# Kernel tuning notes

Measured on AMD Instinct MI355X. Metric: run time of the kernel, lower is better.

The kernel has to match this reference:

```python
import jax, jax.numpy as jnp
import numpy as np

N = 65536      # total nodes (ground + sub)
NG = 32768     # ground nodes (subnodes are NG..N)
H = 64         # n_hidden
FIN = 32       # n_node_features
L = 2          # num_convolution_blocks
B = 64         # graphs in batch
MAXDEG = 10    # MFConv max_degree -> 11 buckets
EG = 1048576   # ground-graph edges
ES = 1048576   # subgraph edges
EX = 524288    # cross (ground<->sub) edges


def setup_inputs() -> dict:
    key = jax.random.key(0)
    ks = jax.random.split(key, 32)
    NS = N - NG
    x = jax.random.normal(ks[0], (N, FIN), jnp.float32)
    # ground graph: src/dst in [0, NG)
    edge_index = jax.random.randint(ks[1], (2, EG), 0, NG).astype(jnp.int64)
    # subgraph: src/dst in [NG, N)
    subgraph_edge_index = (NG + jax.random.randint(ks[2], (2, ES), 0, NS)).astype(jnp.int64)
    # ground -> sub
    ns_src = jax.random.randint(ks[3], (EX,), 0, NG)
    ns_dst = NG + jax.random.randint(ks[4], (EX,), 0, NS)
    node_subnode_index = jnp.stack([ns_src, ns_dst]).astype(jnp.int64)
    # sub -> ground
    sn_src = NG + jax.random.randint(ks[5], (EX,), 0, NS)
    sn_dst = jax.random.randint(ks[6], (EX,), 0, NG)
    subnode_node_index = jnp.stack([sn_src, sn_dst]).astype(jnp.int64)
    ground_node = jnp.arange(N) < NG
    subgraph_batch_index = jax.random.randint(ks[7], (N,), 0, B).astype(jnp.int64)
    batch_idx = jax.random.randint(ks[8], (N,), 0, B).astype(jnp.int64)
    s = 0.05
    p = {}
    p['embed_W'] = jax.random.normal(ks[9], (FIN, H), jnp.float32) * s
    p['embed_b'] = jnp.zeros((H,), jnp.float32)
    names = ['ground', 'g2s', 'sub', 's2g']
    for i, nm in enumerate(names):
        p[nm + '_Wl'] = jax.random.normal(ks[10 + 3 * i], (L, MAXDEG + 1, H, H), jnp.float32) * s
        p[nm + '_bl'] = jnp.zeros((L, MAXDEG + 1, H), jnp.float32)
        p[nm + '_Wr'] = jax.random.normal(ks[11 + 3 * i], (L, MAXDEG + 1, H, H), jnp.float32) * s
    p['W1'] = jax.random.normal(ks[24], (H, H), jnp.float32) * s
    p['b1'] = jnp.zeros((H,), jnp.float32)
    p['W2'] = jax.random.normal(ks[25], (H, 1), jnp.float32) * s
    p['b2'] = jnp.zeros((1,), jnp.float32)
    return dict(x=x, edge_index=edge_index, subgraph_edge_index=subgraph_edge_index,
                node_subnode_index=node_subnode_index, subnode_node_index=subnode_node_index,
                ground_node=ground_node, subgraph_batch_index=subgraph_batch_index,
                batch_idx=batch_idx, **p)


def _mfconv(h, src, dst, Wl, bl, Wr):
    # PyG MFConv: out_i = Lin_l[deg_i](sum_{j->i} h_j) + Lin_r[deg_i](h_i), deg clamped to MAXDEG
    n = h.shape[0]
    deg = jnp.clip(jax.ops.segment_sum(jnp.ones(src.shape[0], jnp.int32), dst, num_segments=n), 0, MAXDEG)
    agg = jax.ops.segment_sum(h[src], dst, num_segments=n)  # [n, H] sum aggregation
    out = jnp.zeros((n, Wl.shape[-1]), h.dtype)
    for d in range(MAXDEG + 1):
        m = (deg == d)[:, None]
        out = out + jnp.where(m, agg @ Wl[d] + bl[d] + h @ Wr[d], jnp.zeros((), h.dtype))
    return out


def _masked_conv(h, ei, Wl, bl, Wr):
    # nodes that never receive a message keep their old features (catch_lone_sender)
    src, dst = ei[0], ei[1]
    recv = jnp.zeros((h.shape[0],), bool).at[dst].set(True)
    return jnp.where(recv[:, None], _mfconv(h, src, dst, Wl, bl, Wr), h)


def reference(x, edge_index, subgraph_edge_index, node_subnode_index, subnode_node_index,
              ground_node, subgraph_batch_index, batch_idx,
              embed_W, embed_b,
              ground_Wl, ground_bl, ground_Wr,
              g2s_Wl, g2s_bl, g2s_Wr,
              sub_Wl, sub_bl, sub_Wr,
              s2g_Wl, s2g_bl, s2g_Wr,
              W1, b1, W2, b2):
    h = x @ embed_W + embed_b
    for l in range(L):
        if l > 0:
            h = jax.nn.relu(h)
        h = _masked_conv(h, edge_index, ground_Wl[l], ground_bl[l], ground_Wr[l])
        h = _masked_conv(h, node_subnode_index, g2s_Wl[l], g2s_bl[l], g2s_Wr[l])
        h = _masked_conv(h, subgraph_edge_index, sub_Wl[l], sub_bl[l], sub_Wr[l])
        h = _masked_conv(h, subnode_node_index, s2g_Wl[l], s2g_bl[l], s2g_Wr[l])
    # global_add_pool over ground nodes only
    pooled = jax.ops.segment_sum(jnp.where(ground_node[:, None], h, jnp.zeros((), h.dtype)),
                                 batch_idx, num_segments=B)  # [B, H]
    z = jax.nn.relu(pooled @ W1 + b1)
    return z @ W2 + b2  # [B, 1]
```

## Files before the change

kernel.cpp:

```cpp
#include <hip/hip_runtime.h>

#define N_NODES 65536
#define NGROUND 32768
#define NHALF 32768
#define H 64
#define FIN 32
#define NB 64
#define MAXDEG 10
#define RSTRIDE 32769
#define EG 1048576
#define ES 1048576
#define EX 524288
#define TE (EG + EX + ES + EX)
#define BIN2 512
#define NPB 64
#define CHUNK 8192
#define TC 384
#define CNT_LEN 196608
#define NSCANB 192
#define BCAP 6144
#define NEB 2048
#define NFB 32
#define ESTR 80

typedef __attribute__((ext_vector_type(8))) short short8;
typedef __attribute__((ext_vector_type(4))) float f32x4;
typedef unsigned short u16;
typedef unsigned int u32;

__device__ __forceinline__ u16 f2bf(float x) {
    unsigned int u = __float_as_uint(x);
    unsigned int r = u + 0x7FFFu + ((u >> 16) & 1u);
    return (u16)(r >> 16);
}
__device__ __forceinline__ float bf2f(u16 b) {
    return __uint_as_float(((unsigned int)b) << 16);
}
__device__ __forceinline__ u32 relu2(u32 w) {
    u32 lo = w & 0xFFFFu;
    if (lo & 0x8000u) lo = 0;
    u32 hi = w >> 16;
    if (hi & 0x8000u) hi = 0;
    return lo | (hi << 16);
}

__device__ __forceinline__ void chunk_resolve(int b, int& set, int& cin,
                                              int& nc, int& base, int& dbase, int& sbase) {
    if (b < 128)      { set = 0; cin = b;       nc = 128; base = 0;      dbase = 0;       sbase = 0; }
    else if (b < 192) { set = 1; cin = b - 128; nc = 64;  base = 65536;  dbase = NGROUND; sbase = 0; }
    else if (b < 320) { set = 2; cin = b - 192; nc = 128; base = 98304;  dbase = NGROUND; sbase = NGROUND; }
    else              { set = 3; cin = b - 320; nc = 64;  base = 163840; dbase = 0;       sbase = NGROUND; }
}

__global__ __launch_bounds__(256) void embed_prep_count_kernel(
    const float* __restrict__ x, const float* __restrict__ W,
    const float* __restrict__ b, u16* __restrict__ hgHi, u16* __restrict__ hsHi,
    const float* W0l, const float* W0r, const float* W1l, const float* W1r,
    const float* W2l, const float* W2r, const float* W3l, const float* W3r,
    short8* __restrict__ fragbuf,
    const int* __restrict__ d0, const int* __restrict__ d1,
    const int* __restrict__ d2, const int* __restrict__ d3,
    int* __restrict__ cnt) {
    int tid = threadIdx.x;
    if (blockIdx.x >= NEB + NFB) {
        __shared__ int hist[BIN2];
        int set, cin, nc, base, dbase, sbase;
        chunk_resolve(blockIdx.x - NEB - NFB, set, cin, nc, base, dbase, sbase);
        const int* dp = set == 0 ? d0 : set == 1 ? d1 : set == 2 ? d2 : d3;
        for (int i = tid; i < BIN2; i += 256) hist[i] = 0;
        __syncthreads();
        int e0 = cin * CHUNK;
        for (int i = tid; i < CHUNK; i += 256) {
            int d = __builtin_nontemporal_load(&dp[e0 + i]) - dbase;
            atomicAdd(&hist[d >> 6], 1);
        }
        __syncthreads();
        for (int i = tid; i < BIN2; i += 256)
            cnt[base + i * nc + cin] = hist[i];
        return;
    }
    if (blockIdx.x >= NEB) {
        int tid2 = (blockIdx.x - NEB) * 256 + tid;
        int lane = tid2 & 63;
        int f8 = (tid2 >> 6) & 7;
        int mat = (tid2 >> 9) & 1;
        int layer = (tid2 >> 10) & 1;
        int set = (tid2 >> 11) & 3;
        int s = f8 >> 2, t = f8 & 3;
        const float* Wb;
        if (set == 0) Wb = mat ? W0r : W0l;
        else if (set == 1) Wb = mat ? W1r : W1l;
        else if (set == 2) Wb = mat ? W2r : W2l;
        else Wb = mat ? W3r : W3l;
        Wb += ((size_t)layer * (MAXDEG + 1) + MAXDEG) * H * H;
        int k0 = s * 32 + (lane >> 4) * 8;
        int n = t * 16 + (lane & 15);
        short8 hi, lo;
#pragma unroll
        for (int j = 0; j < 8; j++) {
            float w = Wb[(size_t)(k0 + j) * H + n];
            u16 hb = f2bf(w);
            u16 lb = f2bf(w - bf2f(hb));
            hi[j] = (short)hb;
            lo[j] = (short)lb;
        }
        size_t basehi = ((size_t)(((set * 2 + layer) * 2 + mat) * 2 + 0) * 8 + f8) * 64 + lane;
        size_t baselo = ((size_t)(((set * 2 + layer) * 2 + mat) * 2 + 1) * 8 + f8) * 64 + lane;
        fragbuf[basehi] = hi;
        fragbuf[baselo] = lo;
        return;
    }
    int f = tid & 63;
    int wy = tid >> 6;
    __shared__ float sW[FIN * H];
    for (int i = tid; i < FIN * H; i += 256) sW[i] = W[i];
    __syncthreads();
    float bf_ = b[f];
#pragma unroll
    for (int it = 0; it < 8; it++) {
        int node = blockIdx.x * 32 + it * 4 + wy;
        const float* xr = x + (size_t)node * FIN;
        float acc = bf_;
#pragma unroll
        for (int k = 0; k < FIN; k++) acc += xr[k] * sW[k * H + f];
        if (node < NGROUND)
            hgHi[(size_t)node * H + f] = f2bf(acc);
        else
            hsHi[(size_t)(node - NGROUND) * H + f] = f2bf(acc);
    }
}

__global__ __launch_bounds__(256) void scanA_kernel(
    int* __restrict__ cnt, int* __restrict__ bsum) {
    __shared__ int lds[256];
    int t = threadIdx.x;
    int base = blockIdx.x * 1024 + t * 4;
    int v0 = cnt[base], v1 = cnt[base + 1], v2 = cnt[base + 2], v3 = cnt[base + 3];
    int s = v0 + v1 + v2 + v3;
    lds[t] = s;
    __syncthreads();
    for (int d = 1; d < 256; d <<= 1) {
        int x = 0;
        if (t >= d) x = lds[t - d];
        __syncthreads();
        lds[t] += x;
        __syncthreads();
    }
    int pref = lds[t] - s;
    cnt[base] = pref;
    cnt[base + 1] = pref + v0;
    cnt[base + 2] = pref + v0 + v1;
    cnt[base + 3] = pref + v0 + v1 + v2;
    if (t == 255) bsum[blockIdx.x] = pref + s;
}

__global__ __launch_bounds__(256) void scanB_kernel(int* __restrict__ bsum) {
    __shared__ int lds[256];
    int t = threadIdx.x;
    int v = (t < NSCANB) ? bsum[t] : 0;
    lds[t] = v;
    __syncthreads();
    for (int d = 1; d < 256; d <<= 1) {
        int x = 0;
        if (t >= d) x = lds[t - d];
        __syncthreads();
        lds[t] += x;
        __syncthreads();
    }
    if (t < NSCANB) bsum[t] = lds[t] - v;
}

__global__ __launch_bounds__(256) void partition_kernel(
    const int* __restrict__ s0, const int* __restrict__ s1,
    const int* __restrict__ s2, const int* __restrict__ s3,
    const int* __restrict__ d0, const int* __restrict__ d1,
    const int* __restrict__ d2, const int* __restrict__ d3,
    const int* __restrict__ cnt, const int* __restrict__ bsum,
    u32* __restrict__ csru) {
    __shared__ u32 buf[CHUNK];
    __shared__ int hist[BIN2];
    __shared__ int lofs[BIN2];
    __shared__ int gbase[BIN2];
    __shared__ int sc[256];
    int set, cin, nc, base, dbase, sbase;
    chunk_resolve(blockIdx.x, set, cin, nc, base, dbase, sbase);
    const int* dp = set == 0 ? d0 : set == 1 ? d1 : set == 2 ? d2 : d3;
    const int* sp = set == 0 ? s0 : set == 1 ? s1 : set == 2 ? s2 : s3;
    int t = threadIdx.x;
    for (int i = t; i < BIN2; i += 256) hist[i] = 0;
    __syncthreads();
    u32 pk[32];
    int e0 = cin * CHUNK;
#pragma unroll
    for (int j = 0; j < 32; j++) {
        int idx = e0 + t + j * 256;
        int d = __builtin_nontemporal_load(&dp[idx]) - dbase;
        int s = __builtin_nontemporal_load(&sp[idx]) - sbase;
        pk[j] = ((u32)d << 15) | (u32)s;
        atomicAdd(&hist[d >> 6], 1);
    }
    __syncthreads();
    int h0 = hist[2 * t], h1 = hist[2 * t + 1];
    int hs = h0 + h1;
    sc[t] = hs;
    __syncthreads();
    for (int d2 = 1; d2 < 256; d2 <<= 1) {
        int v = 0;
        if (t >= d2) v = sc[t - d2];
        __syncthreads();
        sc[t] += v;
        __syncthreads();
    }
    int pref = sc[t] - hs;
    lofs[2 * t] = pref;
    lofs[2 * t + 1] = pref + h0;
    hist[2 * t] = pref;
    hist[2 * t + 1] = pref + h0;
    for (int i = t; i < BIN2; i += 256) {
        int idx = base + i * nc + cin;
        gbase[i] = cnt[idx] + bsum[idx >> 10];
    }
    __syncthreads();
#pragma unroll
    for (int j = 0; j < 32; j++) {
        int bin = pk[j] >> 21;
        int pos = atomicAdd(&hist[bin], 1);
        buf[pos] = pk[j];
    }
    __syncthreads();
    for (int i = t; i < CHUNK; i += 256) {
        u32 pkt = buf[i];
        int d = pkt >> 15;
        int bin = d >> 6;
        int gpos = gbase[bin] + (i - lofs[bin]);
        csru[gpos] = pkt & 0x1FFFFFu;
    }
}

__global__ __launch_bounds__(256) void finalize_kernel(
    u32* __restrict__ csru, const int* __restrict__ cnt,
    const int* __restrict__ bsum, int* __restrict__ rowstart4) {
    __shared__ u32 buf[BCAP];
    __shared__ int deg[NPB], off[NPB];
    int b = blockIdx.x;
    int set = b >> 9, bin = b & 511;
    int nc = (set == 0 || set == 2) ? 128 : 64;
    int base = set == 0 ? 0 : set == 1 ? 65536 : set == 2 ? 98304 : 163840;
    int flat = base + bin * nc;
    int binstart = cnt[flat] + bsum[flat >> 10];
    int binend = (b == 2047) ? TE : (cnt[flat + nc] + bsum[(flat + nc) >> 10]);
    int n = binend - binstart;
    for (int i = threadIdx.x; i < n; i += 256) buf[i] = csru[binstart + i];
    if (threadIdx.x < NPB) deg[threadIdx.x] = 0;
    __syncthreads();
    for (int i = threadIdx.x; i < n; i += 256) atomicAdd(&deg[buf[i] >> 15], 1);
    __syncthreads();
    if (threadIdx.x == 0) {
        int r = 0;
        for (int j = 0; j < NPB; j++) { off[j] = r; r += deg[j]; }
    }
    __syncthreads();
    int coffset = set == 0 ? 0 : set == 1 ? EG : set == 2 ? EG + EX : EG + EX + ES;
    if (threadIdx.x < NPB)
        rowstart4[set * RSTRIDE + bin * NPB + threadIdx.x] =
            binstart - coffset + off[threadIdx.x];
    if (bin == 0 && threadIdx.x == 0)
        rowstart4[set * RSTRIDE + NHALF] = (set == 0 || set == 2) ? EG : EX;
    if (threadIdx.x < NPB) deg[threadIdx.x] = off[threadIdx.x];
    __syncthreads();
    for (int i = threadIdx.x; i < n; i += 256) {
        u32 pkt = buf[i];
        int dl = pkt >> 15;
        int pos = atomicAdd(&deg[dl], 1);
        csru[binstart + pos] = pkt & 0x7FFFu;
    }
}

__global__ __launch_bounds__(256) void conv_fused_kernel(
    const u16* __restrict__ srcHi, const u16* __restrict__ selfHi,
    u16* __restrict__ outHi, const int* __restrict__ csr,
    const int* __restrict__ rowstart, const short8* __restrict__ fragbase,
    const float* __restrict__ Wlp, const float* __restrict__ Wrp,
    const float* __restrict__ blp, int do_relu, u32* __restrict__ relu_buf) {
    if (blockIdx.x >= 2048) {
        int base = ((blockIdx.x - 2048) * 256 + threadIdx.x) * 2;
        uint4* p = (uint4*)relu_buf;
        uint4 a = p[base], b = p[base + 1];
        a.x = relu2(a.x); a.y = relu2(a.y); a.z = relu2(a.z); a.w = relu2(a.w);
        b.x = relu2(b.x); b.y = relu2(b.y); b.z = relu2(b.z); b.w = relu2(b.w);
        p[base] = a;
        p[base + 1] = b;
        return;
    }
    __shared__ u16 sB[H][ESTR];
    __shared__ float sAgg[16][68];
    int tid = threadIdx.x;
    int w = tid >> 6, lane = tid & 63;
    int node0 = blockIdx.x * 16;
    int q = lane >> 4, mrow = lane & 15;

    int R0 = rowstart[node0];
    int R16 = rowstart[node0 + 16];
    int rlo = rowstart[node0 + mrow];
    int rhi = rowstart[node0 + mrow + 1];
    u32 rspan = (u32)(rhi - rlo);

    f32x4 aggv = (f32x4){0.f, 0.f, 0.f, 0.f};

    int el = lane;
    int fh = w;
    for (int ce = R0; ce < R16; ce += 64) {
        int eg = ce + el;
        int src = csr[min(eg, R16 - 1)];
        const uint4* rp = (const uint4*)(srcHi + (size_t)src * H + fh * 16);
        uint4 va = rp[0];
        uint4 vb = rp[1];
        __syncthreads();
        u32 wa[4] = {va.x, va.y, va.z, va.w};
        u32 wb[4] = {vb.x, vb.y, vb.z, vb.w};
#pragma unroll
        for (int k = 0; k < 4; k++) {
            sB[fh * 16 + 2 * k][el] = (u16)wa[k];
            sB[fh * 16 + 2 * k + 1][el] = (u16)(wa[k] >> 16);
            sB[fh * 16 + 8 + 2 * k][el] = (u16)wb[k];
            sB[fh * 16 + 8 + 2 * k + 1][el] = (u16)(wb[k] >> 16);
        }
        __syncthreads();
#pragma unroll
        for (int half = 0; half < 2; half++) {
            int kb = ce + half * 32 + q * 8;
            short8 Af;
#pragma unroll
            for (int j = 0; j < 8; j++) {
                u32 off = (u32)(kb + j) - (u32)rlo;
                Af[j] = (off < rspan) ? (short)0x3F80 : (short)0;
            }
            short8 Bf = *(const short8*)&sB[w * 16 + mrow][half * 32 + q * 8];
            aggv = __builtin_amdgcn_mfma_f32_16x16x32_bf16(Af, Bf, aggv, 0, 0, 0);
        }
    }
#pragma unroll
    for (int r = 0; r < 4; r++) sAgg[q * 4 + r][w * 16 + mrow] = aggv[r];
    __syncthreads();

    int myrow = node0 + mrow;
    int mydeg = rhi - rlo;
    unsigned long long ball = __ballot(min(mydeg, MAXDEG) != MAXDEG);
    unsigned exc = (unsigned)(ball & 0xFFFFull);
    int t = w;

    f32x4 accv = (f32x4){0.f, 0.f, 0.f, 0.f};
    const short8* fb = fragbase + lane;
#pragma unroll
    for (int s = 0; s < 2; s++) {
        float av[8];
        *(float4*)&av[0] = *(const float4*)&sAgg[mrow][s * 32 + q * 8];
        *(float4*)&av[4] = *(const float4*)&sAgg[mrow][s * 32 + q * 8 + 4];
        short8 Ahi;
#pragma unroll
        for (int j = 0; j < 8; j++) Ahi[j] = (short)f2bf(av[j]);
        short8 Hhi = *(const short8*)(selfHi + (size_t)myrow * H + s * 32 + q * 8);
        short8 BLhi = fb[(size_t)((0 * 8) + s * 4 + t) * 64];
        short8 BLlo = fb[(size_t)((1 * 8) + s * 4 + t) * 64];
        short8 BRhi = fb[(size_t)((2 * 8) + s * 4 + t) * 64];
        short8 BRlo = fb[(size_t)((3 * 8) + s * 4 + t) * 64];
        accv = __builtin_amdgcn_mfma_f32_16x16x32_bf16(Ahi, BLhi, accv, 0, 0, 0);
        accv = __builtin_amdgcn_mfma_f32_16x16x32_bf16(Ahi, BLlo, accv, 0, 0, 0);
        accv = __builtin_amdgcn_mfma_f32_16x16x32_bf16(Hhi, BRhi, accv, 0, 0, 0);
        accv = __builtin_amdgcn_mfma_f32_16x16x32_bf16(Hhi, BRlo, accv, 0, 0, 0);
    }

    {
        int n = t * 16 + mrow;
        float bv = blp[MAXDEG * H + n];
#pragma unroll
        for (int r = 0; r < 4; r++) {
            int mm = q * 4 + r;
            if (!((exc >> mm) & 1)) {
                float val = accv[r] + bv;
                if (do_relu) val = fmaxf(val, 0.f);
                outHi[(size_t)(node0 + mm) * H + n] = f2bf(val);
            }
        }
    }

    if (exc & (0xFu << (w * 4))) {
        for (int i = 0; i < 4; i++) {
            int nr = w * 4 + i;
            if (!((exc >> nr) & 1)) continue;
            int node = node0 + nr;
            int st = rowstart[node], en = rowstart[node + 1];
            int dg = en - st;
            if (dg == 0) {
                float v = bf2f(selfHi[(size_t)node * H + lane]);
                if (do_relu) v = fmaxf(v, 0.f);
                outHi[(size_t)node * H + lane] = f2bf(v);
            } else {
                int d = min(dg, MAXDEG);
                const float* wl = Wlp + (size_t)d * H * H;
                const float* wr = Wrp + (size_t)d * H * H;
                float sval = bf2f(selfHi[(size_t)node * H + lane]);
                float o = blp[d * H + lane];
#pragma unroll 4
                for (int k = 0; k < H; k++) {
                    o += sAgg[nr][k] * wl[k * H + lane];
                    o += __shfl(sval, k, 64) * wr[k * H + lane];
                }
                if (do_relu) o = fmaxf(o, 0.f);
                outHi[(size_t)node * H + lane] = f2bf(o);
            }
        }
    }
}

__global__ __launch_bounds__(256) void pool_kernel(
    const u16* __restrict__ hgHi, const int* __restrict__ batch_idx,
    float* __restrict__ pooled) {
    __shared__ float lp[NB * H];
    int tid = threadIdx.x;
    for (int i = tid; i < NB * H; i += 256) lp[i] = 0.f;
    __syncthreads();
    int f = tid & 63;
    int wave = tid >> 6;
    int start = blockIdx.x * 64;
    for (int n = wave; n < 64; n += 4) {
        int node = start + n;
        int bi = batch_idx[node];
        atomicAdd(&lp[bi * H + f], bf2f(hgHi[(size_t)node * H + f]));
    }
    __syncthreads();
    for (int i = tid; i < NB * H; i += 256) {
        float v = lp[i];
        if (v != 0.f) atomicAdd(&pooled[i], v);
    }
}

__global__ __launch_bounds__(64) void mlp_kernel(
    const float* __restrict__ pooled, const float* __restrict__ W1,
    const float* __restrict__ b1, const float* __restrict__ W2,
    const float* __restrict__ b2, float* __restrict__ out) {
    int b = blockIdx.x;
    int j = threadIdx.x;
    const float* pr = pooled + b * H;
    float acc = b1[j];
#pragma unroll
    for (int k = 0; k < H; k++) acc += pr[k] * W1[k * H + j];
    acc = fmaxf(acc, 0.f);
    float v = acc * W2[j];
#pragma unroll
    for (int off = 32; off > 0; off >>= 1) v += __shfl_down(v, off, 64);
    if (j == 0) out[b] = v + b2[0];
}

extern "C" void kernel_launch(void* const* d_in, const int* in_sizes, int n_in,
                              void* d_out, int out_size, void* d_ws, size_t ws_size,
                              hipStream_t stream) {
    const float* x = (const float*)d_in[0];
    const int* ei_ground = (const int*)d_in[1];
    const int* ei_sub = (const int*)d_in[2];
    const int* ei_g2s = (const int*)d_in[3];
    const int* ei_s2g = (const int*)d_in[4];
    const int* batch_idx = (const int*)d_in[7];
    const float* embed_W = (const float*)d_in[8];
    const float* embed_b = (const float*)d_in[9];
    const float* Wl[4] = {(const float*)d_in[10], (const float*)d_in[13],
                          (const float*)d_in[16], (const float*)d_in[19]};
    const float* bl[4] = {(const float*)d_in[11], (const float*)d_in[14],
                          (const float*)d_in[17], (const float*)d_in[20]};
    const float* Wr[4] = {(const float*)d_in[12], (const float*)d_in[15],
                          (const float*)d_in[18], (const float*)d_in[21]};
    const float* W1 = (const float*)d_in[22];
    const float* b1 = (const float*)d_in[23];
    const float* W2 = (const float*)d_in[24];
    const float* b2 = (const float*)d_in[25];

    const int* s_[4] = {ei_ground, ei_g2s, ei_sub, ei_s2g};
    const int* dsr[4] = {ei_ground + EG, ei_g2s + EX, ei_sub + ES, ei_s2g + EX};
    const size_t coff[4] = {0, (size_t)EG, (size_t)EG + EX, (size_t)EG + EX + ES};

    const size_t HB = (size_t)NHALF * H * sizeof(u16);
    char* p = (char*)d_ws;
    u16* hgHi[2] = {(u16*)p, (u16*)(p + HB)};            p += 2 * HB;
    u16* hsHi[2] = {(u16*)p, (u16*)(p + HB)};            p += 2 * HB;
    u32* csru = (u32*)p;           p += (size_t)TE * sizeof(u32);
    int* cnt = (int*)p;            p += (size_t)CNT_LEN * sizeof(int);
    int* bsum = (int*)p;           p += (size_t)NSCANB * sizeof(int);
    int* rowstart4 = (int*)p;      p += (size_t)4 * RSTRIDE * sizeof(int);
    p += 16 - ((size_t)p & 15);
    short8* fragbuf = (short8*)p;  p += (size_t)8192 * sizeof(short8);
    float* pooled = (float*)p;

    embed_prep_count_kernel<<<NEB + NFB + TC, 256, 0, stream>>>(
        x, embed_W, embed_b, hgHi[0], hsHi[0],
        Wl[0], Wr[0], Wl[1], Wr[1], Wl[2], Wr[2], Wl[3], Wr[3], fragbuf,
        dsr[0], dsr[1], dsr[2], dsr[3], cnt);

    scanA_kernel<<<NSCANB, 256, 0, stream>>>(cnt, bsum);
    scanB_kernel<<<1, 256, 0, stream>>>(bsum);
    partition_kernel<<<TC, 256, 0, stream>>>(
        s_[0], s_[1], s_[2], s_[3], dsr[0], dsr[1], dsr[2], dsr[3], cnt, bsum, csru);
    finalize_kernel<<<2048, 256, 0, stream>>>(csru, cnt, bsum, rowstart4);
    const int* csr = (const int*)csru;

    int cg = 0, cs = 0;
    for (int l = 0; l < 2; l++) {
        for (int c = 0; c < 4; c++) {
            const u16 *srcHi, *selfHi;
            u16 *outHi;
            if (c == 0)      { srcHi = hgHi[cg]; selfHi = hgHi[cg]; outHi = hgHi[1 - cg]; }
            else if (c == 1) { srcHi = hgHi[cg]; selfHi = hsHi[cs]; outHi = hsHi[1 - cs]; }
            else if (c == 2) { srcHi = hsHi[cs]; selfHi = hsHi[cs]; outHi = hsHi[1 - cs]; }
            else             { srcHi = hsHi[cs]; selfHi = hgHi[cg]; outHi = hgHi[1 - cg]; }
            int do_relu = (l == 0 && c == 3) ? 1 : 0;
            int relu_blocks = (l == 1 && c == 0) ? 512 : 0;
            u32* relu_buf = (l == 1 && c == 0) ? (u32*)hsHi[cs] : (u32*)nullptr;
            conv_fused_kernel<<<2048 + relu_blocks, 256, 0, stream>>>(
                srcHi, selfHi, outHi,
                csr + coff[c], rowstart4 + (size_t)c * RSTRIDE,
                fragbuf + (size_t)(c * 2 + l) * 2048,
                Wl[c] + (size_t)l * (MAXDEG + 1) * H * H,
                Wr[c] + (size_t)l * (MAXDEG + 1) * H * H,
                bl[c] + (size_t)l * (MAXDEG + 1) * H, do_relu, relu_buf);
            if (c == 0 || c == 3) cg ^= 1; else cs ^= 1;
        }
    }

    hipMemsetAsync(pooled, 0, (size_t)NB * H * sizeof(float), stream);
    pool_kernel<<<NGROUND / 64, 256, 0, stream>>>(hgHi[cg], batch_idx, pooled);
    mlp_kernel<<<NB, 64, 0, stream>>>(pooled, W1, b1, W2, b2, (float*)d_out);
}
```

Baseline: 410.9 us.

## Double-buffer edge gather in conv kernel and replace pool atomics with partials

The conv aggregation loop now prefetches the next chunk's source indices and feature rows into registers while the current chunk is processed, and uses a double-buffered shared tile so only one barrier is needed per chunk. The shared row stride changes from 80 to 72. Pooling drops the memset and global atomics: 128 blocks each write a per-block partial, and the MLP kernel sums those partials before its matmul. This adds register pressure and shared memory in the conv kernel and extra partial-buffer traffic in the MLP.

```diff
diff --git a/kernel.cpp b/kernel.cpp
--- a/kernel.cpp
+++ b/kernel.cpp
@@ -21,7 +21,8 @@
 #define BCAP 6144
 #define NEB 2048
 #define NFB 32
-#define ESTR 80
+#define ESTR 72
+#define NPOOLB 128
 
 typedef __attribute__((ext_vector_type(8))) short short8;
 typedef __attribute__((ext_vector_type(4))) float f32x4;
@@ -292,7 +293,7 @@
         p[base + 1] = b;
         return;
     }
-    __shared__ u16 sB[H][ESTR];
+    __shared__ u16 sB[2][H][ESTR];
     __shared__ float sAgg[16][68];
     int tid = threadIdx.x;
     int w = tid >> 6, lane = tid & 63;
@@ -309,23 +310,32 @@
 
     int el = lane;
     int fh = w;
-    for (int ce = R0; ce < R16; ce += 64) {
-        int eg = ce + el;
-        int src = csr[min(eg, R16 - 1)];
-        const uint4* rp = (const uint4*)(srcHi + (size_t)src * H + fh * 16);
-        uint4 va = rp[0];
-        uint4 vb = rp[1];
-        __syncthreads();
-        u32 wa[4] = {va.x, va.y, va.z, va.w};
-        u32 wb[4] = {vb.x, vb.y, vb.z, vb.w};
+    int nch = (R16 - R0 + 63) >> 6;
+    int egb = R0 + el;
+
+    int sc_ = csr[min(egb, R16 - 1)];
+    const uint4* rp0 = (const uint4*)(srcHi + (size_t)sc_ * H + fh * 16);
+    uint4 va_c = rp0[0];
+    uint4 vb_c = rp0[1];
+    int sn_ = csr[min(egb + 64, R16 - 1)];
+
+    for (int t = 0; t < nch; t++) {
+        int cur = t & 1;
+        u32 wa[4] = {va_c.x, va_c.y, va_c.z, va_c.w};
+        u32 wb[4] = {vb_c.x, vb_c.y, vb_c.z, vb_c.w};
 #pragma unroll
         for (int k = 0; k < 4; k++) {
-            sB[fh * 16 + 2 * k][el] = (u16)wa[k];
-            sB[fh * 16 + 2 * k + 1][el] = (u16)(wa[k] >> 16);
-            sB[fh * 16 + 8 + 2 * k][el] = (u16)wb[k];
-            sB[fh * 16 + 8 + 2 * k + 1][el] = (u16)(wb[k] >> 16);
-        }
-        __syncthreads();
+            sB[cur][fh * 16 + 2 * k][el] = (u16)wa[k];
+            sB[cur][fh * 16 + 2 * k + 1][el] = (u16)(wa[k] >> 16);
+            sB[cur][fh * 16 + 8 + 2 * k][el] = (u16)wb[k];
+            sB[cur][fh * 16 + 8 + 2 * k + 1][el] = (u16)(wb[k] >> 16);
+        }
+        const uint4* rpn = (const uint4*)(srcHi + (size_t)sn_ * H + fh * 16);
+        uint4 va_n = rpn[0];
+        uint4 vb_n = rpn[1];
+        int sn2_ = csr[min(egb + (t + 2) * 64, R16 - 1)];
+        __syncthreads();
+        int ce = R0 + (t << 6);
 #pragma unroll
         for (int half = 0; half < 2; half++) {
             int kb = ce + half * 32 + q * 8;
@@ -335,9 +345,10 @@
                 u32 off = (u32)(kb + j) - (u32)rlo;
                 Af[j] = (off < rspan) ? (short)0x3F80 : (short)0;
             }
-            short8 Bf = *(const short8*)&sB[w * 16 + mrow][half * 32 + q * 8];
+            short8 Bf = *(const short8*)&sB[cur][w * 16 + mrow][half * 32 + q * 8];
             aggv = __builtin_amdgcn_mfma_f32_16x16x32_bf16(Af, Bf, aggv, 0, 0, 0);
         }
+        va_c = va_n; vb_c = vb_n; sn_ = sn2_;
     }
 #pragma unroll
     for (int r = 0; r < 4; r++) sAgg[q * 4 + r][w * 16 + mrow] = aggv[r];
@@ -415,33 +426,36 @@
 
 __global__ __launch_bounds__(256) void pool_kernel(
     const u16* __restrict__ hgHi, const int* __restrict__ batch_idx,
-    float* __restrict__ pooled) {
+    float* __restrict__ partials) {
     __shared__ float lp[NB * H];
     int tid = threadIdx.x;
     for (int i = tid; i < NB * H; i += 256) lp[i] = 0.f;
     __syncthreads();
     int f = tid & 63;
     int wave = tid >> 6;
-    int start = blockIdx.x * 64;
-    for (int n = wave; n < 64; n += 4) {
+    int start = blockIdx.x * (NGROUND / NPOOLB);
+    for (int n = wave; n < NGROUND / NPOOLB; n += 4) {
         int node = start + n;
         int bi = batch_idx[node];
         atomicAdd(&lp[bi * H + f], bf2f(hgHi[(size_t)node * H + f]));
     }
     __syncthreads();
-    for (int i = tid; i < NB * H; i += 256) {
-        float v = lp[i];
-        if (v != 0.f) atomicAdd(&pooled[i], v);
-    }
+    float* op = partials + (size_t)blockIdx.x * (NB * H);
+    for (int i = tid; i < NB * H; i += 256) op[i] = lp[i];
 }
 
 __global__ __launch_bounds__(64) void mlp_kernel(
-    const float* __restrict__ pooled, const float* __restrict__ W1,
+    const float* __restrict__ partials, const float* __restrict__ W1,
     const float* __restrict__ b1, const float* __restrict__ W2,
     const float* __restrict__ b2, float* __restrict__ out) {
     int b = blockIdx.x;
     int j = threadIdx.x;
-    const float* pr = pooled + b * H;
+    float p_ = 0.f;
+    for (int g = 0; g < NPOOLB; g++)
+        p_ += partials[(size_t)g * (NB * H) + b * H + j];
+    __shared__ float pr[H];
+    pr[j] = p_;
+    __syncthreads();
     float acc = b1[j];
 #pragma unroll
     for (int k = 0; k < H; k++) acc += pr[k] * W1[k * H + j];
@@ -488,7 +502,7 @@
     int* rowstart4 = (int*)p;      p += (size_t)4 * RSTRIDE * sizeof(int);
     p += 16 - ((size_t)p & 15);
     short8* fragbuf = (short8*)p;  p += (size_t)8192 * sizeof(short8);
-    float* pooled = (float*)p;
+    float* partials = (float*)p;
 
     embed_prep_count_kernel<<<NEB + NFB + TC, 256, 0, stream>>>(
         x, embed_W, embed_b, hgHi[0], hsHi[0],
@@ -525,7 +539,6 @@
         }
     }
 
-    hipMemsetAsync(pooled, 0, (size_t)NB * H * sizeof(float), stream);
-    pool_kernel<<<NGROUND / 64, 256, 0, stream>>>(hgHi[cg], batch_idx, pooled);
-    mlp_kernel<<<NB, 64, 0, stream>>>(pooled, W1, b1, W2, b2, (float*)d_out);
-}
+    pool_kernel<<<NPOOLB, 256, 0, stream>>>(hgHi[cg], batch_idx, partials);
+    mlp_kernel<<<NB, 64, 0, stream>>>(partials, W1, b1, W2, b2, (float*)d_out);
+}
```

After: 430.5 us. +4.8%, slower.
